# Optimization experiments

Measured on AMD Instinct MI355X. Metric: run time of the kernel, lower is better.

## Reference

```python
import jax, jax.numpy as jnp
import numpy as np

L, B, D = 512, 16, 256
H = 4            # MAX_DIFF == num_heads
MAX_BONDS = 6
MAX_DIFF = 4
PROB_SHIFT = 0.3


def _attn_weights(x, Wqk, Wq, bq, Wk, bk, mask):
    """Per-head softmax(QK^T/sqrt(hd)) with key padding mask.
    x: [b,l,d]; Wqk: [d,2d] (the inc/dec_qk pre-projection);
    Wq/Wk: [d,d] (MHA in_proj, stored x@W layout); mask: [b,l] bool (True=masked).
    Returns [b,h,l,l]. The V path / out_proj of the torch MHA are discarded
    by the original module, so they are omitted here.
    """
    b, l, d = x.shape
    hd = d // H
    q = x @ Wqk[:, :d]
    k = x @ Wqk[:, d:]
    Q = (q @ Wq + bq).reshape(b, l, H, hd)
    K = (k @ Wk + bk).reshape(b, l, H, hd)
    scores = jnp.einsum('blhd,bmhd->bhlm', Q, K) / np.sqrt(hd)
    scores = jnp.where(mask[:, None, None, :], -jnp.inf, scores)
    return jax.nn.softmax(scores, axis=-1)


def setup_inputs() -> dict:
    key = jax.random.key(0)
    ks = jax.random.split(key, 16)
    s = 0.05
    p = lambda k, shape: jax.random.normal(k, shape, jnp.float32) * s
    # key_padding_mask: last 64 positions padded (True == masked)
    src_mask = jnp.broadcast_to(jnp.arange(L)[None, :] >= (L - 64), (B, L))
    return {
        'molecule_embedding': jax.random.normal(ks[0], (L, B, D), jnp.float32),
        'src_bond': jax.random.randint(ks[1], (B, L, MAX_BONDS), 0, L, jnp.int32),
        'src_mask': src_mask,
        'W_inc_qk': p(ks[2], (D, 2 * D)),
        'Wq_inc': p(ks[3], (D, D)), 'bq_inc': p(ks[4], (D,)),
        'Wk_inc': p(ks[5], (D, D)), 'bk_inc': p(ks[6], (D,)),
        'W_dec_qk': p(ks[7], (D, 2 * D)),
        'Wq_dec': p(ks[8], (D, D)), 'bq_dec': p(ks[9], (D,)),
        'Wk_dec': p(ks[10], (D, D)), 'bk_dec': p(ks[11], (D,)),
        'Wc': p(ks[12], (MAX_DIFF, MAX_DIFF)), 'bc': p(ks[13], (MAX_DIFF,)),
    }


def reference(molecule_embedding, src_bond, src_mask,
              W_inc_qk, Wq_inc, bq_inc, Wk_inc, bk_inc,
              W_dec_qk, Wq_dec, bq_dec, Wk_dec, bk_dec,
              Wc, bc):
    x = jnp.transpose(molecule_embedding, (1, 0, 2))  # [b,l,d]
    b, l, _ = x.shape

    inc = _attn_weights(x, W_inc_qk, Wq_inc, bq_inc, Wk_inc, bk_inc, src_mask)
    dec = _attn_weights(x, W_dec_qk, Wq_dec, bq_dec, Wk_dec, bk_dec, src_mask)

    pad = (~src_mask).astype(jnp.float32)              # 1 - mask
    pm2 = pad[:, :, None] * pad[:, None, :]            # [b,l,l]

    # cls_layer((inc-dec).permute(0,2,3,1)) * (MAX_DIFF*pad_mask)[...,None]
    diff = (jnp.einsum('bhlm,hc->blmc', inc - dec, Wc) + bc)
    diff = diff * (MAX_DIFF * pm2)[..., None]          # [b,l,l,4]

    # src_bond has last dim == MAX_BONDS -> one-hot neighbor counts
    src_w = jax.nn.one_hot(src_bond, l, dtype=jnp.float32).sum(axis=2) * pm2  # [b,l,l]
    eye = jnp.eye(l, dtype=jnp.float32)
    src_w = src_w * (1.0 - eye)[None]                  # zero diagonal

    # _shift_probs(src_weight.long(), prob_shift, MAX_DIFF)
    oh = jax.nn.one_hot(src_w.astype(jnp.int32), MAX_DIFF, dtype=jnp.float32)
    probs = oh * (1.0 - PROB_SHIFT) + (1.0 - oh) * (PROB_SHIFT / (MAX_DIFF - 1))
    probs = probs / probs.sum(axis=-1, keepdims=True)

    return jnp.log(probs + 1e-6) + diff                # [b,l,l,4]
```

## Files before the change

kernel.cpp:

```cpp
#include <hip/hip_runtime.h>
#include <stdint.h>

typedef unsigned short u16t;
typedef short s8v __attribute__((ext_vector_type(8)));
typedef float f4v __attribute__((ext_vector_type(4)));

#define MFMA16 __builtin_amdgcn_mfma_f32_16x16x32_bf16
#define QKN (16*4*512*64)

__device__ __forceinline__ u16t f2bf(float f) {
  unsigned u = __builtin_bit_cast(unsigned, f);
  u += 0x7fffu + ((u >> 16) & 1u);
  return (u16t)(u >> 16);
}

__global__ __launch_bounds__(256) void prep_kernel(
    const float* __restrict__ Wiqk, const float* __restrict__ Wqi, const float* __restrict__ Wki,
    const float* __restrict__ Wdqk, const float* __restrict__ Wqd, const float* __restrict__ Wkd,
    u16t* __restrict__ weffT, const int* __restrict__ mraw, int* __restrict__ mdst) {
  __shared__ float At[16][65];
  __shared__ float Bt[16][65];
  __shared__ int mode;
  const int tid = threadIdx.x;

  if (blockIdx.z == 4) {
    if (tid == 0) mode = 0;
    __syncthreads();
    unsigned v0 = (unsigned)mraw[tid], v1 = (unsigned)mraw[tid + 256];
    if (v0 == 0x3F800000u || v1 == 0x3F800000u) mode = 2;
    __syncthreads();
    if (mode == 0 && (v0 > 1u || v1 > 1u)) mode = 1;
    __syncthreads();
    const int g = blockIdx.y * 4 + blockIdx.x;
#pragma unroll
    for (int i = 0; i < 2; ++i) {
      int idx = g * 512 + i * 256 + tid;
      int m;
      if (mode == 2)      m = (((const float*)mraw)[idx] != 0.0f) ? 1 : 0;
      else if (mode == 1) m = ((const unsigned char*)mraw)[idx];
      else                m = mraw[idx];
      mdst[idx] = m;
    }
    return;
  }

  const int n0 = blockIdx.x * 64;
  const int d0 = blockIdx.y * 64;
  const int p  = blockIdx.z;
  const float* A2  = (p == 0) ? Wqi : (p == 1) ? Wki : (p == 2) ? Wqd : Wkd;
  const float* Wqk = (p < 2) ? Wiqk : Wdqk;
  const int aoff = (p & 1) * 256;
  const int tx = tid & 15, ty = tid >> 4;

  float acc[4][4];
#pragma unroll
  for (int i = 0; i < 4; ++i)
#pragma unroll
    for (int j = 0; j < 4; ++j) acc[i][j] = 0.f;

  for (int k0 = 0; k0 < 256; k0 += 16) {
    __syncthreads();
    {
      int nn = tid & 63, kr = tid >> 6;
#pragma unroll
      for (int pass = 0; pass < 4; ++pass) {
        int kk = kr + pass * 4;
        At[kk][nn] = A2[(size_t)(k0 + kk) * 256 + n0 + nn];
      }
      int kk = tid & 15, dr = tid >> 4;
#pragma unroll
      for (int pass = 0; pass < 4; ++pass) {
        int dd = dr + pass * 16;
        Bt[kk][dd] = Wqk[(size_t)(d0 + dd) * 512 + aoff + k0 + kk];
      }
    }
    __syncthreads();
#pragma unroll
    for (int kk = 0; kk < 16; ++kk) {
      float a[4], b[4];
#pragma unroll
      for (int i = 0; i < 4; ++i) a[i] = At[kk][ty * 4 + i];
#pragma unroll
      for (int j = 0; j < 4; ++j) b[j] = Bt[kk][tx * 4 + j];
#pragma unroll
      for (int i = 0; i < 4; ++i)
#pragma unroll
        for (int j = 0; j < 4; ++j) acc[i][j] = fmaf(a[i], b[j], acc[i][j]);
    }
  }

#pragma unroll
  for (int i = 0; i < 4; ++i) {
    u16t h[4] = {f2bf(acc[i][0]), f2bf(acc[i][1]), f2bf(acc[i][2]), f2bf(acc[i][3])};
    *(uint2*)(&weffT[((size_t)(p * 256 + n0 + ty * 4 + i)) * 256 + d0 + tx * 4]) =
        *(const uint2*)h;
  }
}

__global__ __launch_bounds__(256) void proj_kernel(
    const float* __restrict__ emb, const u16t* __restrict__ weffT,
    const float* __restrict__ bq_inc, const float* __restrict__ bk_inc,
    const float* __restrict__ bq_dec, const float* __restrict__ bk_dec,
    u16t* __restrict__ qk) {
  __shared__ __align__(16) u16t As[128 * 40];
  __shared__ __align__(16) u16t Bs[128 * 40];
  const int t = threadIdx.x;
  const int n0 = blockIdx.x * 128;
  const int r0 = blockIdx.y * 128;
  const int bb = r0 >> 9;
  const int l0 = r0 & 511;
  const int lane = t & 63, wid = t >> 6;
  const int quad = lane >> 4, c15 = lane & 15;
  const int wm = wid >> 1, wn = wid & 1;

  f4v acc[4][4];
#pragma unroll
  for (int i = 0; i < 4; ++i)
#pragma unroll
    for (int j = 0; j < 4; ++j) acc[i][j] = f4v{0.f, 0.f, 0.f, 0.f};

  for (int k0 = 0; k0 < 256; k0 += 32) {
    __syncthreads();
#pragma unroll
    for (int i = 0; i < 2; ++i) {
      int c = t + i * 256;
      int m = c >> 2, off = (c & 3) * 8;
      const float* src = emb + (size_t)((l0 + m) * 16 + bb) * 256 + k0 + off;
      float4 x0 = *(const float4*)src;
      float4 x1 = *(const float4*)(src + 4);
      u16t h[8] = {f2bf(x0.x), f2bf(x0.y), f2bf(x0.z), f2bf(x0.w),
                   f2bf(x1.x), f2bf(x1.y), f2bf(x1.z), f2bf(x1.w)};
      *(uint4*)(&As[m * 40 + off]) = *(const uint4*)h;
      *(uint4*)(&Bs[m * 40 + off]) =
          *(const uint4*)(weffT + (size_t)(n0 + m) * 256 + k0 + off);
    }
    __syncthreads();
    s8v af[4], bf[4];
#pragma unroll
    for (int mi = 0; mi < 4; ++mi)
      af[mi] = *(const s8v*)(&As[(wm * 64 + mi * 16 + c15) * 40 + quad * 8]);
#pragma unroll
    for (int ni = 0; ni < 4; ++ni)
      bf[ni] = *(const s8v*)(&Bs[(wn * 64 + ni * 16 + c15) * 40 + quad * 8]);
#pragma unroll
    for (int mi = 0; mi < 4; ++mi)
#pragma unroll
      for (int ni = 0; ni < 4; ++ni)
        acc[mi][ni] = MFMA16(af[mi], bf[ni], acc[mi][ni], 0, 0, 0);
  }

  const float* biasP[4] = {bq_inc, bk_inc, bq_dec, bk_dec};
#pragma unroll
  for (int ni = 0; ni < 4; ++ni) {
    int n = n0 + wn * 64 + ni * 16 + c15;
    int p = n >> 8, h = (n >> 6) & 3, tt = n & 63, jj = n & 255;
    float bias = biasP[p][jj];
    u16t* dst = qk + (size_t)p * QKN;
#pragma unroll
    for (int mi = 0; mi < 4; ++mi) {
#pragma unroll
      for (int reg = 0; reg < 4; ++reg) {
        int l = l0 + wm * 64 + mi * 16 + quad * 4 + reg;
        dst[((size_t)(bb * 4 + h) * 512 + l) * 64 + tt] = f2bf(acc[mi][ni][reg] + bias);
      }
    }
  }
}

__global__ __launch_bounds__(512) void fused_kernel(
    const u16t* __restrict__ qk, const int* __restrict__ mask,
    const int* __restrict__ src_bond, const float* __restrict__ Wc,
    const float* __restrict__ bc, float* __restrict__ out) {
  __shared__ __align__(16) u16t Qs[8 * 16 * 72];
  __shared__ int bondsL[96];
  __shared__ int mlds[512 + 16];
  __shared__ __align__(16) float rpart[2][16][8];
  __shared__ float wlds[16];
  const int t = threadIdx.x;

  const int f = (int)(blockIdx.x + gridDim.x * blockIdx.y);
  const int j = f >> 3;
  const int bb = (f & 7) * 2 + (j >> 5);
  const int l0 = (j & 31) * 16;

#pragma unroll
  for (int i = 0; i < 2; ++i) {
    int c = t + i * 512;
    int q = c >> 7, row = (c >> 3) & 15, off = (c & 7) * 8;
    const u16t* Qb = qk + (size_t)(2 * (q >> 2)) * QKN;
    *(uint4*)(&Qs[(q * 16 + row) * 72 + off]) =
        *(const uint4*)(Qb + ((size_t)(bb * 4 + (q & 3)) * 512 + l0 + row) * 64 + off);
  }
  mlds[t] = mask[bb * 512 + t];
  if (t < 16) mlds[512 + t] = mask[bb * 512 + l0 + t];
  if (t < 96) bondsL[t] = src_bond[(size_t)(bb * 512 + l0 + t / 6) * 6 + (t % 6)];
  if (t >= 96 && t < 112) wlds[t - 96] = Wc[t - 96];

  const int lane = t & 63, wid = t >> 6;
  const int quad = lane >> 4, c15 = lane & 15;
  const int mbase = wid * 64 + c15;

  float dacc[4][4][4];
#pragma unroll
  for (int nt = 0; nt < 4; ++nt)
#pragma unroll
    for (int r = 0; r < 4; ++r)
#pragma unroll
      for (int c = 0; c < 4; ++c) dacc[nt][r][c] = 0.f;

  s8v kb0[4], kb1[4];
  {
    const u16t* Kb = qk + (size_t)1 * QKN + (size_t)(bb * 4 + 0) * 512 * 64;
#pragma unroll
    for (int nt = 0; nt < 4; ++nt) {
      const u16t* row = Kb + (size_t)(mbase + nt * 16) * 64 + quad * 8;
      kb0[nt] = *(const s8v*)row;
      kb1[nt] = *(const s8v*)(row + 32);
    }
  }

  __syncthreads();

  bool mskm[4];
#pragma unroll
  for (int nt = 0; nt < 4; ++nt) mskm[nt] = (mlds[mbase + nt * 16] != 0);

#pragma unroll 1
  for (int q = 0; q < 8; ++q) {
    const int pp = q >> 2, h = q & 3;
    s8v a0 = *(const s8v*)(&Qs[(q * 16 + c15) * 72 + quad * 8]);
    s8v a1 = *(const s8v*)(&Qs[(q * 16 + c15) * 72 + 32 + quad * 8]);

    float wv[4];
#pragma unroll
    for (int c = 0; c < 4; ++c) wv[c] = wlds[h * 4 + c];

    float E[4][4];
    float rsum[4] = {0.f, 0.f, 0.f, 0.f};
#pragma unroll
    for (int nt = 0; nt < 4; ++nt) {
      f4v sacc = f4v{0.f, 0.f, 0.f, 0.f};
      sacc = MFMA16(a0, kb0[nt], sacc, 0, 0, 0);
      sacc = MFMA16(a1, kb1[nt], sacc, 0, 0, 0);
#pragma unroll
      for (int reg = 0; reg < 4; ++reg) {
        float e = mskm[nt] ? 0.f : __expf(sacc[reg] * 0.125f);
        E[nt][reg] = e;
        rsum[reg] += e;
      }
    }

    if (q < 7) {
      const int qn = q + 1;
      const u16t* Kb = qk + (size_t)(2 * (qn >> 2) + 1) * QKN
                          + (size_t)(bb * 4 + (qn & 3)) * 512 * 64;
#pragma unroll
      for (int nt = 0; nt < 4; ++nt) {
        const u16t* row = Kb + (size_t)(mbase + nt * 16) * 64 + quad * 8;
        kb0[nt] = *(const s8v*)row;
        kb1[nt] = *(const s8v*)(row + 32);
      }
    }

#pragma unroll
    for (int reg = 0; reg < 4; ++reg) {
#pragma unroll
      for (int off = 1; off < 16; off <<= 1) rsum[reg] += __shfl_xor(rsum[reg], off);
    }
    if (c15 == 0) {
#pragma unroll
      for (int reg = 0; reg < 4; ++reg) rpart[q & 1][quad * 4 + reg][wid] = rsum[reg];
    }
    __syncthreads();

    float inv[4];
    const float sgn = pp ? -1.f : 1.f;
#pragma unroll
    for (int reg = 0; reg < 4; ++reg) {
      const float4* rp = (const float4*)&rpart[q & 1][quad * 4 + reg][0];
      float4 s0 = rp[0], s1 = rp[1];
      inv[reg] = sgn / (s0.x + s0.y + s0.z + s0.w + s1.x + s1.y + s1.z + s1.w);
    }

#pragma unroll
    for (int nt = 0; nt < 4; ++nt) {
#pragma unroll
      for (int reg = 0; reg < 4; ++reg) {
        float P = E[nt][reg] * inv[reg];
#pragma unroll
        for (int c = 0; c < 4; ++c)
          dacc[nt][reg][c] = fmaf(P, wv[c], dacc[nt][reg][c]);
      }
    }
  }

  float bcF[4];
#pragma unroll
  for (int c = 0; c < 4; ++c) bcF[c] = bc[c];
  const float lgH = logf(0.7f + 1e-6f);
  const float lgM = logf(0.1f + 1e-6f);
  const float lgU = logf(0.25f + 1e-6f);

#pragma unroll
  for (int nt = 0; nt < 4; ++nt) {
    int m = mbase + nt * 16;
    bool padm = !mskm[nt];
#pragma unroll
    for (int reg = 0; reg < 4; ++reg) {
      int lloc = quad * 4 + reg;
      int l = l0 + lloc;
      bool padl = (mlds[512 + lloc] == 0);
      bool pm = padl && padm;
      int cnt = 0;
#pragma unroll
      for (int j6 = 0; j6 < 6; ++j6) cnt += (bondsL[lloc * 6 + j6] == m) ? 1 : 0;
      int cls = (pm && (m != l)) ? cnt : 0;
      float v[4];
#pragma unroll
      for (int c = 0; c < 4; ++c) {
        float lp = (cls >= 4) ? lgU : ((c == cls) ? lgH : lgM);
        float dv = pm ? 4.f * (dacc[nt][reg][c] + bcF[c]) : 0.f;
        v[c] = lp + dv;
      }
      float4 o = make_float4(v[0], v[1], v[2], v[3]);
      *(float4*)(&out[((size_t)(bb * 512 + l) * 512 + m) * 4]) = o;
    }
  }
}

extern "C" void kernel_launch(void* const* d_in, const int* in_sizes, int n_in,
                              void* d_out, int out_size, void* d_ws, size_t ws_size,
                              hipStream_t stream) {
  (void)in_sizes; (void)n_in; (void)out_size; (void)ws_size;
  const float* emb      = (const float*)d_in[0];
  const int*   src_bond = (const int*)d_in[1];
  const int*   mask_raw = (const int*)d_in[2];
  const float* W_inc_qk = (const float*)d_in[3];
  const float* Wq_inc   = (const float*)d_in[4];
  const float* bq_inc   = (const float*)d_in[5];
  const float* Wk_inc   = (const float*)d_in[6];
  const float* bk_inc   = (const float*)d_in[7];
  const float* W_dec_qk = (const float*)d_in[8];
  const float* Wq_dec   = (const float*)d_in[9];
  const float* bq_dec   = (const float*)d_in[10];
  const float* Wk_dec   = (const float*)d_in[11];
  const float* bk_dec   = (const float*)d_in[12];
  const float* Wc       = (const float*)d_in[13];
  const float* bc       = (const float*)d_in[14];
  float* out = (float*)d_out;

  char* ws = (char*)d_ws;
  int*   wsMask = (int*)ws;
  u16t*  weffT  = (u16t*)(ws + 32768);
  u16t*  qk     = (u16t*)(ws + 32768 + 524288);

  hipLaunchKernelGGL(prep_kernel, dim3(4, 4, 5), dim3(256), 0, stream,
                     W_inc_qk, Wq_inc, Wk_inc, W_dec_qk, Wq_dec, Wk_dec, weffT,
                     mask_raw, wsMask);
  hipLaunchKernelGGL(proj_kernel, dim3(8, 64), dim3(256), 0, stream,
                     emb, weffT, bq_inc, bk_inc, bq_dec, bk_dec, qk);
  hipLaunchKernelGGL(fused_kernel, dim3(32, 16), dim3(512), 0, stream,
                     qk, wsMask, src_bond, Wc, bc, out);
}
```

Measured before the change: 175.1 us.

## Recompute scores in second pass to drop per-head sync and cut registers

The fused kernel now makes two passes. The first computes QK scores only to gather the softmax row sums, with no per-head barrier. After a single reduction into shared inverse sums, a second pass recomputes the scores per column tile and accumulates the class projection there, so the 64-float dacc array across all tiles is no longer held in registers, and launch bounds ask for 4 blocks per CU. The projection kernel also remaps block indices so rows are grouped per XCD for cache locality. The cost is doubled MFMA and exp work plus K reloads from global memory in the second pass.

Measured after the change: 232.7 us. +32.9%, slower.

```diff
diff --git a/kernel.cpp b/kernel.cpp
--- a/kernel.cpp
+++ b/kernel.cpp
@@ -105,8 +105,12 @@
   __shared__ __align__(16) u16t As[128 * 40];
   __shared__ __align__(16) u16t Bs[128 * 40];
   const int t = threadIdx.x;
-  const int n0 = blockIdx.x * 128;
-  const int r0 = blockIdx.y * 128;
+  const int f = (int)(blockIdx.x + gridDim.x * blockIdx.y);
+  const int xcd = f & 7, idx = f >> 3;
+  const int ry = xcd * 8 + (idx & 7);
+  const int nx = idx >> 3;
+  const int n0 = nx * 128;
+  const int r0 = ry * 128;
   const int bb = r0 >> 9;
   const int l0 = r0 & 511;
   const int lane = t & 63, wid = t >> 6;
@@ -167,21 +171,25 @@
   }
 }
 
-__global__ __launch_bounds__(512) void fused_kernel(
+__global__ __launch_bounds__(512, 4) void fused_kernel(
     const u16t* __restrict__ qk, const int* __restrict__ mask,
     const int* __restrict__ src_bond, const float* __restrict__ Wc,
     const float* __restrict__ bc, float* __restrict__ out) {
   __shared__ __align__(16) u16t Qs[8 * 16 * 72];
   __shared__ int bondsL[96];
   __shared__ int mlds[512 + 16];
-  __shared__ __align__(16) float rpart[2][16][8];
-  __shared__ float wlds[16];
+  __shared__ __align__(16) float rpart[8][16][8];
+  __shared__ __align__(16) float invL[8][16];
   const int t = threadIdx.x;
 
   const int f = (int)(blockIdx.x + gridDim.x * blockIdx.y);
   const int j = f >> 3;
   const int bb = (f & 7) * 2 + (j >> 5);
   const int l0 = (j & 31) * 16;
+
+  const int lane = t & 63, wid = t >> 6;
+  const int quad = lane >> 4, c15 = lane & 15;
+  const int mbase = wid * 64 + c15;
 
 #pragma unroll
   for (int i = 0; i < 2; ++i) {
@@ -194,23 +202,10 @@
   mlds[t] = mask[bb * 512 + t];
   if (t < 16) mlds[512 + t] = mask[bb * 512 + l0 + t];
   if (t < 96) bondsL[t] = src_bond[(size_t)(bb * 512 + l0 + t / 6) * 6 + (t % 6)];
-  if (t >= 96 && t < 112) wlds[t - 96] = Wc[t - 96];
-
-  const int lane = t & 63, wid = t >> 6;
-  const int quad = lane >> 4, c15 = lane & 15;
-  const int mbase = wid * 64 + c15;
-
-  float dacc[4][4][4];
-#pragma unroll
-  for (int nt = 0; nt < 4; ++nt)
-#pragma unroll
-    for (int r = 0; r < 4; ++r)
-#pragma unroll
-      for (int c = 0; c < 4; ++c) dacc[nt][r][c] = 0.f;
 
   s8v kb0[4], kb1[4];
   {
-    const u16t* Kb = qk + (size_t)1 * QKN + (size_t)(bb * 4 + 0) * 512 * 64;
+    const u16t* Kb = qk + (size_t)1 * QKN + (size_t)(bb * 4) * 512 * 64;
 #pragma unroll
     for (int nt = 0; nt < 4; ++nt) {
       const u16t* row = Kb + (size_t)(mbase + nt * 16) * 64 + quad * 8;
@@ -227,27 +222,16 @@
 
 #pragma unroll 1
   for (int q = 0; q < 8; ++q) {
-    const int pp = q >> 2, h = q & 3;
     s8v a0 = *(const s8v*)(&Qs[(q * 16 + c15) * 72 + quad * 8]);
     s8v a1 = *(const s8v*)(&Qs[(q * 16 + c15) * 72 + 32 + quad * 8]);
 
-    float wv[4];
-#pragma unroll
-    for (int c = 0; c < 4; ++c) wv[c] = wlds[h * 4 + c];
-
-    float E[4][4];
-    float rsum[4] = {0.f, 0.f, 0.f, 0.f};
+    f4v s[4];
 #pragma unroll
     for (int nt = 0; nt < 4; ++nt) {
       f4v sacc = f4v{0.f, 0.f, 0.f, 0.f};
       sacc = MFMA16(a0, kb0[nt], sacc, 0, 0, 0);
       sacc = MFMA16(a1, kb1[nt], sacc, 0, 0, 0);
-#pragma unroll
-      for (int reg = 0; reg < 4; ++reg) {
-        float e = mskm[nt] ? 0.f : __expf(sacc[reg] * 0.125f);
-        E[nt][reg] = e;
-        rsum[reg] += e;
-      }
+      s[nt] = sacc;
     }
 
     if (q < 7) {
@@ -262,6 +246,13 @@
       }
     }
 
+    float rsum[4] = {0.f, 0.f, 0.f, 0.f};
+#pragma unroll
+    for (int nt = 0; nt < 4; ++nt) {
+#pragma unroll
+      for (int reg = 0; reg < 4; ++reg)
+        rsum[reg] += mskm[nt] ? 0.f : __expf(s[nt][reg] * 0.125f);
+    }
 #pragma unroll
     for (int reg = 0; reg < 4; ++reg) {
 #pragma unroll
@@ -269,48 +260,74 @@
     }
     if (c15 == 0) {
 #pragma unroll
-      for (int reg = 0; reg < 4; ++reg) rpart[q & 1][quad * 4 + reg][wid] = rsum[reg];
-    }
-    __syncthreads();
-
-    float inv[4];
-    const float sgn = pp ? -1.f : 1.f;
-#pragma unroll
-    for (int reg = 0; reg < 4; ++reg) {
-      const float4* rp = (const float4*)&rpart[q & 1][quad * 4 + reg][0];
-      float4 s0 = rp[0], s1 = rp[1];
-      inv[reg] = sgn / (s0.x + s0.y + s0.z + s0.w + s1.x + s1.y + s1.z + s1.w);
-    }
-
-#pragma unroll
-    for (int nt = 0; nt < 4; ++nt) {
-#pragma unroll
-      for (int reg = 0; reg < 4; ++reg) {
-        float P = E[nt][reg] * inv[reg];
-#pragma unroll
-        for (int c = 0; c < 4; ++c)
-          dacc[nt][reg][c] = fmaf(P, wv[c], dacc[nt][reg][c]);
-      }
-    }
-  }
-
+      for (int reg = 0; reg < 4; ++reg) rpart[q][quad * 4 + reg][wid] = rsum[reg];
+    }
+  }
+
+  __syncthreads();
+
+  if (t < 128) {
+    int q = t >> 4, lr = t & 15;
+    float4 r0 = *(const float4*)&rpart[q][lr][0];
+    float4 r1 = *(const float4*)&rpart[q][lr][4];
+    invL[q][lr] = 1.0f / (r0.x + r0.y + r0.z + r0.w + r1.x + r1.y + r1.z + r1.w);
+  }
+
+  __syncthreads();
+
+  float Wf[16];
+#pragma unroll
+  for (int i = 0; i < 16; ++i) Wf[i] = Wc[i];
   float bcF[4];
 #pragma unroll
   for (int c = 0; c < 4; ++c) bcF[c] = bc[c];
   const float lgH = logf(0.7f + 1e-6f);
   const float lgM = logf(0.1f + 1e-6f);
   const float lgU = logf(0.25f + 1e-6f);
-
-#pragma unroll
+  bool padl[4];
+  int lcls[4];
+#pragma unroll
+  for (int reg = 0; reg < 4; ++reg) padl[reg] = (mlds[512 + quad * 4 + reg] == 0);
+
+#pragma unroll 1
   for (int nt = 0; nt < 4; ++nt) {
-    int m = mbase + nt * 16;
+    const int m = mbase + nt * 16;
+    float dacc[4][4];
+#pragma unroll
+    for (int r = 0; r < 4; ++r)
+#pragma unroll
+      for (int c = 0; c < 4; ++c) dacc[r][c] = 0.f;
+
+#pragma unroll
+    for (int q = 0; q < 8; ++q) {
+      const u16t* Kb = qk + (size_t)(2 * (q >> 2) + 1) * QKN
+                          + (size_t)(bb * 4 + (q & 3)) * 512 * 64;
+      const u16t* krow = Kb + (size_t)m * 64 + quad * 8;
+      s8v k0 = *(const s8v*)krow;
+      s8v k1 = *(const s8v*)(krow + 32);
+      s8v a0 = *(const s8v*)(&Qs[(q * 16 + c15) * 72 + quad * 8]);
+      s8v a1 = *(const s8v*)(&Qs[(q * 16 + c15) * 72 + 32 + quad * 8]);
+      f4v sacc = f4v{0.f, 0.f, 0.f, 0.f};
+      sacc = MFMA16(a0, k0, sacc, 0, 0, 0);
+      sacc = MFMA16(a1, k1, sacc, 0, 0, 0);
+      f4v ivv = *(const f4v*)&invL[q][quad * 4];
+#pragma unroll
+      for (int reg = 0; reg < 4; ++reg) {
+        float e = mskm[nt] ? 0.f : __expf(sacc[reg] * 0.125f);
+        float P = e * ivv[reg];
+        if (q >= 4) P = -P;
+#pragma unroll
+        for (int c = 0; c < 4; ++c)
+          dacc[reg][c] = fmaf(P, Wf[(q & 3) * 4 + c], dacc[reg][c]);
+      }
+    }
+
     bool padm = !mskm[nt];
 #pragma unroll
     for (int reg = 0; reg < 4; ++reg) {
       int lloc = quad * 4 + reg;
       int l = l0 + lloc;
-      bool padl = (mlds[512 + lloc] == 0);
-      bool pm = padl && padm;
+      bool pm = padl[reg] && padm;
       int cnt = 0;
 #pragma unroll
       for (int j6 = 0; j6 < 6; ++j6) cnt += (bondsL[lloc * 6 + j6] == m) ? 1 : 0;
@@ -319,13 +336,14 @@
 #pragma unroll
       for (int c = 0; c < 4; ++c) {
         float lp = (cls >= 4) ? lgU : ((c == cls) ? lgH : lgM);
-        float dv = pm ? 4.f * (dacc[nt][reg][c] + bcF[c]) : 0.f;
+        float dv = pm ? 4.f * (dacc[reg][c] + bcF[c]) : 0.f;
         v[c] = lp + dv;
       }
       float4 o = make_float4(v[0], v[1], v[2], v[3]);
       *(float4*)(&out[((size_t)(bb * 512 + l) * 512 + m) * 4]) = o;
     }
   }
+  (void)lcls;
 }
 
 extern "C" void kernel_launch(void* const* d_in, const int* in_sizes, int n_in,
```

## Precompute softmax row sums per wave to remove per-head block barriers

Applied to the files above, without the earlier changes.

The fused kernel first runs a pass in which each wave computes the full softmax denominator for one head/projection pair and stores the inverse in shared memory. This removes the per-iteration __syncthreads and the cross-wave partial-sum exchange from the main loop, at the cost of recomputing the QK scores and exponentials once more. The projection kernel also remaps blocks so neighbouring blocks share the same XCD and row tiles. It converts fp32 to bf16 with the packed hardware instruction instead of software rounding.

After: 201.8 us. 15.2% more time.

```diff
diff --git a/kernel.cpp b/kernel.cpp
--- a/kernel.cpp
+++ b/kernel.cpp
@@ -105,8 +105,12 @@
   __shared__ __align__(16) u16t As[128 * 40];
   __shared__ __align__(16) u16t Bs[128 * 40];
   const int t = threadIdx.x;
-  const int n0 = blockIdx.x * 128;
-  const int r0 = blockIdx.y * 128;
+  const int f = (int)(blockIdx.x + gridDim.x * blockIdx.y);
+  const int xcd = f & 7, idx = f >> 3;
+  const int ry = xcd * 8 + (idx & 7);
+  const int nx = idx >> 3;
+  const int n0 = nx * 128;
+  const int r0 = ry * 128;
   const int bb = r0 >> 9;
   const int l0 = r0 & 511;
   const int lane = t & 63, wid = t >> 6;
@@ -128,9 +132,13 @@
       const float* src = emb + (size_t)((l0 + m) * 16 + bb) * 256 + k0 + off;
       float4 x0 = *(const float4*)src;
       float4 x1 = *(const float4*)(src + 4);
-      u16t h[8] = {f2bf(x0.x), f2bf(x0.y), f2bf(x0.z), f2bf(x0.w),
-                   f2bf(x1.x), f2bf(x1.y), f2bf(x1.z), f2bf(x1.w)};
-      *(uint4*)(&As[m * 40 + off]) = *(const uint4*)h;
+      unsigned p0, p1, p2, p3;
+      asm("v_cvt_pk_bf16_f32 %0, %1, %2" : "=v"(p0) : "v"(x0.x), "v"(x0.y));
+      asm("v_cvt_pk_bf16_f32 %0, %1, %2" : "=v"(p1) : "v"(x0.z), "v"(x0.w));
+      asm("v_cvt_pk_bf16_f32 %0, %1, %2" : "=v"(p2) : "v"(x1.x), "v"(x1.y));
+      asm("v_cvt_pk_bf16_f32 %0, %1, %2" : "=v"(p3) : "v"(x1.z), "v"(x1.w));
+      uint4 pk = make_uint4(p0, p1, p2, p3);
+      *(uint4*)(&As[m * 40 + off]) = pk;
       *(uint4*)(&Bs[m * 40 + off]) =
           *(const uint4*)(weffT + (size_t)(n0 + m) * 256 + k0 + off);
     }
@@ -174,7 +182,7 @@
   __shared__ __align__(16) u16t Qs[8 * 16 * 72];
   __shared__ int bondsL[96];
   __shared__ int mlds[512 + 16];
-  __shared__ __align__(16) float rpart[2][16][8];
+  __shared__ __align__(16) float invL[8][16];
   __shared__ float wlds[16];
   const int t = threadIdx.x;
 
@@ -182,6 +190,10 @@
   const int j = f >> 3;
   const int bb = (f & 7) * 2 + (j >> 5);
   const int l0 = (j & 31) * 16;
+
+  const int lane = t & 63, wid = t >> 6;
+  const int quad = lane >> 4, c15 = lane & 15;
+  const int mbase = wid * 64 + c15;
 
 #pragma unroll
   for (int i = 0; i < 2; ++i) {
@@ -196,21 +208,43 @@
   if (t < 96) bondsL[t] = src_bond[(size_t)(bb * 512 + l0 + t / 6) * 6 + (t % 6)];
   if (t >= 96 && t < 112) wlds[t - 96] = Wc[t - 96];
 
-  const int lane = t & 63, wid = t >> 6;
-  const int quad = lane >> 4, c15 = lane & 15;
-  const int mbase = wid * 64 + c15;
-
-  float dacc[4][4][4];
-#pragma unroll
-  for (int nt = 0; nt < 4; ++nt)
-#pragma unroll
-    for (int r = 0; r < 4; ++r)
-#pragma unroll
-      for (int c = 0; c < 4; ++c) dacc[nt][r][c] = 0.f;
+  __syncthreads();
+
+  {
+    const int q = wid;
+    const int pp = q >> 2, h = q & 3;
+    const u16t* Kb = qk + (size_t)(2 * pp + 1) * QKN + (size_t)(bb * 4 + h) * 512 * 64;
+    s8v a0 = *(const s8v*)(&Qs[(q * 16 + c15) * 72 + quad * 8]);
+    s8v a1 = *(const s8v*)(&Qs[(q * 16 + c15) * 72 + 32 + quad * 8]);
+    float rs[4] = {0.f, 0.f, 0.f, 0.f};
+#pragma unroll 4
+    for (int tt = 0; tt < 32; ++tt) {
+      const u16t* row = Kb + (size_t)(tt * 16 + c15) * 64 + quad * 8;
+      s8v k0 = *(const s8v*)row;
+      s8v k1 = *(const s8v*)(row + 32);
+      f4v s = f4v{0.f, 0.f, 0.f, 0.f};
+      s = MFMA16(a0, k0, s, 0, 0, 0);
+      s = MFMA16(a1, k1, s, 0, 0, 0);
+      bool msk = (mlds[tt * 16 + c15] != 0);
+#pragma unroll
+      for (int reg = 0; reg < 4; ++reg)
+        rs[reg] += msk ? 0.f : __expf(s[reg] * 0.125f);
+    }
+#pragma unroll
+    for (int reg = 0; reg < 4; ++reg) {
+#pragma unroll
+      for (int off = 1; off < 16; off <<= 1) rs[reg] += __shfl_xor(rs[reg], off);
+    }
+    const float sgn = (q >= 4) ? -1.f : 1.f;
+    if (c15 == 0) {
+#pragma unroll
+      for (int reg = 0; reg < 4; ++reg) invL[q][quad * 4 + reg] = sgn / rs[reg];
+    }
+  }
 
   s8v kb0[4], kb1[4];
   {
-    const u16t* Kb = qk + (size_t)1 * QKN + (size_t)(bb * 4 + 0) * 512 * 64;
+    const u16t* Kb = qk + (size_t)1 * QKN + (size_t)(bb * 4) * 512 * 64;
 #pragma unroll
     for (int nt = 0; nt < 4; ++nt) {
       const u16t* row = Kb + (size_t)(mbase + nt * 16) * 64 + quad * 8;
@@ -225,29 +259,31 @@
 #pragma unroll
   for (int nt = 0; nt < 4; ++nt) mskm[nt] = (mlds[mbase + nt * 16] != 0);
 
+  float dacc[4][4][4];
+#pragma unroll
+  for (int nt = 0; nt < 4; ++nt)
+#pragma unroll
+    for (int r = 0; r < 4; ++r)
+#pragma unroll
+      for (int c = 0; c < 4; ++c) dacc[nt][r][c] = 0.f;
+
 #pragma unroll 1
   for (int q = 0; q < 8; ++q) {
-    const int pp = q >> 2, h = q & 3;
+    const int h = q & 3;
     s8v a0 = *(const s8v*)(&Qs[(q * 16 + c15) * 72 + quad * 8]);
     s8v a1 = *(const s8v*)(&Qs[(q * 16 + c15) * 72 + 32 + quad * 8]);
-
+    f4v ivv = *(const f4v*)&invL[q][quad * 4];
     float wv[4];
 #pragma unroll
     for (int c = 0; c < 4; ++c) wv[c] = wlds[h * 4 + c];
 
-    float E[4][4];
-    float rsum[4] = {0.f, 0.f, 0.f, 0.f};
+    f4v s[4];
 #pragma unroll
     for (int nt = 0; nt < 4; ++nt) {
       f4v sacc = f4v{0.f, 0.f, 0.f, 0.f};
       sacc = MFMA16(a0, kb0[nt], sacc, 0, 0, 0);
       sacc = MFMA16(a1, kb1[nt], sacc, 0, 0, 0);
-#pragma unroll
-      for (int reg = 0; reg < 4; ++reg) {
-        float e = mskm[nt] ? 0.f : __expf(sacc[reg] * 0.125f);
-        E[nt][reg] = e;
-        rsum[reg] += e;
-      }
+      s[nt] = sacc;
     }
 
     if (q < 7) {
@@ -263,30 +299,11 @@
     }
 
 #pragma unroll
-    for (int reg = 0; reg < 4; ++reg) {
-#pragma unroll
-      for (int off = 1; off < 16; off <<= 1) rsum[reg] += __shfl_xor(rsum[reg], off);
-    }
-    if (c15 == 0) {
-#pragma unroll
-      for (int reg = 0; reg < 4; ++reg) rpart[q & 1][quad * 4 + reg][wid] = rsum[reg];
-    }
-    __syncthreads();
-
-    float inv[4];
-    const float sgn = pp ? -1.f : 1.f;
-#pragma unroll
-    for (int reg = 0; reg < 4; ++reg) {
-      const float4* rp = (const float4*)&rpart[q & 1][quad * 4 + reg][0];
-      float4 s0 = rp[0], s1 = rp[1];
-      inv[reg] = sgn / (s0.x + s0.y + s0.z + s0.w + s1.x + s1.y + s1.z + s1.w);
-    }
-
-#pragma unroll
     for (int nt = 0; nt < 4; ++nt) {
 #pragma unroll
       for (int reg = 0; reg < 4; ++reg) {
-        float P = E[nt][reg] * inv[reg];
+        float e = mskm[nt] ? 0.f : __expf(s[nt][reg] * 0.125f);
+        float P = e * ivv[reg];
 #pragma unroll
         for (int c = 0; c < 4; ++c)
           dacc[nt][reg][c] = fmaf(P, wv[c], dacc[nt][reg][c]);
```
